# Kernel tuning notes

Measured on AMD Instinct MI355X. Metric: run time of the kernel, lower is better.

The kernel has to match this reference:

```python
import jax, jax.numpy as jnp
import numpy as np

BETA = 0.1
NUM_LAYERS = 2  # GT layers inside each FastGTN


def densify(edge_index, edge_weight, num_nodes):
    # edge_index: [T, 2, E] int, edge_weight: [T, E] -> dense [T, N, N]
    T, _, E = edge_index.shape
    t_ids = jnp.broadcast_to(jnp.arange(T)[:, None], (T, E))
    dense = jnp.zeros((T, num_nodes, num_nodes), dtype=edge_weight.dtype)
    return dense.at[t_ids, edge_index[:, 0, :], edge_index[:, 1, :]].add(edge_weight)


def fast_gtn(dense_A, X, Ws, conv_w, lin_w, lin_b, num_nodes):
    # Ws: [C, w_in, w_out]; conv_w: [L, C, T]; lin_w: [C*w_out, w_out]
    H = jnp.einsum('nk,ckh->cnh', X, Ws)              # [C, N, w_out]
    X_ = jax.lax.stop_gradient(H)                      # clone().detach()
    for l in range(NUM_LAYERS):
        filt = jax.nn.softmax(conv_w[l], axis=1)       # [C, T]
        adj = jnp.einsum('ct,tij->cij', filt, dense_A) # [C, N, N]
        H = jnp.einsum('cij,cjh->cih', adj, H)         # graph conv per channel
    H_ = jax.nn.relu(BETA * X_ + (1.0 - BETA) * H)     # [C, N, w_out]
    H_ = jnp.transpose(H_, (1, 0, 2)).reshape(num_nodes, -1)  # [N, C*w_out]
    return jax.nn.relu(H_ @ lin_w + lin_b)             # [N, w_out]


def setup_inputs() -> dict:
    key = jax.random.key(0)
    ks = jax.random.split(key, 12)
    T, E, N = 4, 131072, 4096
    C, F_IN, H_OUT = 2, 128, 64
    edge_index = jax.random.randint(ks[0], (T, 2, E), 0, N, dtype=jnp.int64)
    edge_weight = jax.random.uniform(ks[1], (T, E), dtype=jnp.float32)
    X = jax.random.normal(ks[2], (N, F_IN), dtype=jnp.float32)
    def glorot(k, shape):
        fan_in, fan_out = shape[-2], shape[-1]
        s = jnp.sqrt(6.0 / (fan_in + fan_out))
        return jax.random.uniform(k, shape, jnp.float32, -s, s)
    # FastGTN #1 (w_in=F_IN)
    Ws1 = glorot(ks[3], (C, F_IN, H_OUT))
    conv_w1 = 0.1 * jax.random.normal(ks[4], (NUM_LAYERS, C, T), dtype=jnp.float32)
    lin_w1 = glorot(ks[5], (C * H_OUT, H_OUT))
    lin_b1 = jnp.zeros((H_OUT,), jnp.float32)
    # FastGTN #2 (w_in=H_OUT)
    Ws2 = glorot(ks[6], (C, H_OUT, H_OUT))
    conv_w2 = 0.1 * jax.random.normal(ks[7], (NUM_LAYERS, C, T), dtype=jnp.float32)
    lin_w2 = glorot(ks[8], (C * H_OUT, H_OUT))
    lin_b2 = jnp.zeros((H_OUT,), jnp.float32)
    return {"edge_index": edge_index, "edge_weight": edge_weight, "X": X,
            "Ws1": Ws1, "conv_w1": conv_w1, "lin_w1": lin_w1, "lin_b1": lin_b1,
            "Ws2": Ws2, "conv_w2": conv_w2, "lin_w2": lin_w2, "lin_b2": lin_b2}


def reference(edge_index, edge_weight, X, Ws1, conv_w1, lin_w1, lin_b1,
              Ws2, conv_w2, lin_w2, lin_b2):
    N = X.shape[0]
    dense_A = densify(edge_index, edge_weight, N)      # [T, N, N]
    H = fast_gtn(dense_A, X, Ws1, conv_w1, lin_w1, lin_b1, N)
    H = fast_gtn(dense_A, H, Ws2, conv_w2, lin_w2, lin_b2, N)
    return H
```

## Files before the change

### kernel.cpp

```cpp
#include <hip/hip_runtime.h>

#define E_EDGES 131072
#define N_NODES 4096
#define HOUT    64
#define NE_TOT  (4 * E_EDGES)
#define CAP     256
#define CSTRIDE 16
#define SC_NBLK 64
#define SC_NTHR 1024
#define SC_EPB  (NE_TOT / SC_NBLK)
#define SC_EPT  (SC_EPB / SC_NTHR)

__device__ __forceinline__ unsigned short f2bf(float x) {
    unsigned u = __float_as_uint(x);
    return (unsigned short)((u + 0x7FFFu + ((u >> 16) & 1u)) >> 16);
}
__device__ __forceinline__ float bf2f(unsigned b) {
    return __uint_as_float(b << 16);
}

__device__ __forceinline__ void softmax4(const float* __restrict__ cw,
                                         int layer, int c, float f[4]) {
#pragma unroll
    for (int t = 0; t < 4; ++t) f[t] = cw[(layer * 2 + c) * 4 + t];
    float m = fmaxf(fmaxf(f[0], f[1]), fmaxf(f[2], f[3]));
    float s = 0.f;
#pragma unroll
    for (int t = 0; t < 4; ++t) { f[t] = expf(f[t] - m); s += f[t]; }
    float inv = 1.0f / s;
#pragma unroll
    for (int t = 0; t < 4; ++t) f[t] *= inv;
}

__device__ __forceinline__ float selw(const float f[4], int t) {
    float a = (t & 1) ? f[1] : f[0];
    float b = (t & 1) ? f[3] : f[2];
    return (t & 2) ? b : a;
}

__device__ __forceinline__ void fma8(float acc[8], float w, uint4 v) {
    acc[0] += w * bf2f(v.x & 0xFFFFu); acc[1] += w * bf2f(v.x >> 16);
    acc[2] += w * bf2f(v.y & 0xFFFFu); acc[3] += w * bf2f(v.y >> 16);
    acc[4] += w * bf2f(v.z & 0xFFFFu); acc[5] += w * bf2f(v.z >> 16);
    acc[6] += w * bf2f(v.w & 0xFFFFu); acc[7] += w * bf2f(v.w >> 16);
}

__device__ __forceinline__ uint4 pack8(const float acc[8]) {
    uint4 r;
    r.x = (unsigned)f2bf(acc[0]) | ((unsigned)f2bf(acc[1]) << 16);
    r.y = (unsigned)f2bf(acc[2]) | ((unsigned)f2bf(acc[3]) << 16);
    r.z = (unsigned)f2bf(acc[4]) | ((unsigned)f2bf(acc[5]) << 16);
    r.w = (unsigned)f2bf(acc[6]) | ((unsigned)f2bf(acc[7]) << 16);
    return r;
}

__device__ __forceinline__ void spmm_row2c(const unsigned* __restrict__ rowe, int len,
                                           const unsigned* __restrict__ H16,
                                           const float f0[4], const float f1[4],
                                           int lane, float a0[8], float a1[8]) {
    int g  = lane >> 3;
    int hq = lane & 7;
#pragma unroll
    for (int j = 0; j < 8; ++j) { a0[j] = 0.f; a1[j] = 0.f; }
    int e = 0;
    for (; e + 32 <= len; e += 32) {
        unsigned r0 = rowe[e + g];
        unsigned r1 = rowe[e + 8 + g];
        unsigned r2 = rowe[e + 16 + g];
        unsigned r3 = rowe[e + 24 + g];
        int   d0 = r0 & 0xFFF, t0 = (r0 >> 12) & 3;
        int   d1 = r1 & 0xFFF, t1 = (r1 >> 12) & 3;
        int   d2 = r2 & 0xFFF, t2 = (r2 >> 12) & 3;
        int   d3 = r3 & 0xFFF, t3 = (r3 >> 12) & 3;
        float w0 = bf2f(r0 >> 16), w1 = bf2f(r1 >> 16);
        float w2 = bf2f(r2 >> 16), w3 = bf2f(r3 >> 16);
        uint4 v00 = ((const uint4*)(H16 + (d0 * 2 + 0) * 32))[hq];
        uint4 v01 = ((const uint4*)(H16 + (d0 * 2 + 1) * 32))[hq];
        uint4 v10 = ((const uint4*)(H16 + (d1 * 2 + 0) * 32))[hq];
        uint4 v11 = ((const uint4*)(H16 + (d1 * 2 + 1) * 32))[hq];
        uint4 v20 = ((const uint4*)(H16 + (d2 * 2 + 0) * 32))[hq];
        uint4 v21 = ((const uint4*)(H16 + (d2 * 2 + 1) * 32))[hq];
        uint4 v30 = ((const uint4*)(H16 + (d3 * 2 + 0) * 32))[hq];
        uint4 v31 = ((const uint4*)(H16 + (d3 * 2 + 1) * 32))[hq];
        fma8(a0, w0 * selw(f0, t0), v00);
        fma8(a1, w0 * selw(f1, t0), v01);
        fma8(a0, w1 * selw(f0, t1), v10);
        fma8(a1, w1 * selw(f1, t1), v11);
        fma8(a0, w2 * selw(f0, t2), v20);
        fma8(a1, w2 * selw(f1, t2), v21);
        fma8(a0, w3 * selw(f0, t3), v30);
        fma8(a1, w3 * selw(f1, t3), v31);
    }
    for (; e + 8 <= len; e += 8) {
        unsigned r0 = rowe[e + g];
        int   d0 = r0 & 0xFFF, t0 = (r0 >> 12) & 3;
        float w0 = bf2f(r0 >> 16);
        uint4 v00 = ((const uint4*)(H16 + (d0 * 2 + 0) * 32))[hq];
        uint4 v01 = ((const uint4*)(H16 + (d0 * 2 + 1) * 32))[hq];
        fma8(a0, w0 * selw(f0, t0), v00);
        fma8(a1, w0 * selw(f1, t0), v01);
    }
    if (g < len - e) {
        unsigned r0 = rowe[e + g];
        int   d0 = r0 & 0xFFF, t0 = (r0 >> 12) & 3;
        float w0 = bf2f(r0 >> 16);
        uint4 v00 = ((const uint4*)(H16 + (d0 * 2 + 0) * 32))[hq];
        uint4 v01 = ((const uint4*)(H16 + (d0 * 2 + 1) * 32))[hq];
        fma8(a0, w0 * selw(f0, t0), v00);
        fma8(a1, w0 * selw(f1, t0), v01);
    }
#pragma unroll
    for (int j = 0; j < 8; ++j) {
        a0[j] += __shfl_xor(a0[j], 8);
        a0[j] += __shfl_xor(a0[j], 16);
        a0[j] += __shfl_xor(a0[j], 32);
        a1[j] += __shfl_xor(a1[j], 8);
        a1[j] += __shfl_xor(a1[j], 16);
        a1[j] += __shfl_xor(a1[j], 32);
    }
}

__global__ void __launch_bounds__(256)
zinit_kernel(const float* __restrict__ X, const float* __restrict__ Ws,
             float* __restrict__ H0, unsigned* __restrict__ H016,
             int* __restrict__ cursor) {
    int idx = blockIdx.x * 256 + threadIdx.x;
    if (idx < N_NODES * CSTRIDE) cursor[idx] = 0;
    int h = idx & 63;
    int n = (idx >> 6) & (N_NODES - 1);
    int c = idx >> 18;
    const float4* xv = (const float4*)(X + n * 128);
    const float*  w  = Ws + c * 128 * HOUT + h;
    float acc = 0.f;
#pragma unroll 8
    for (int k4 = 0; k4 < 32; ++k4) {
        float4 xx = xv[k4];
        acc += xx.x * w[(k4 * 4 + 0) * HOUT];
        acc += xx.y * w[(k4 * 4 + 1) * HOUT];
        acc += xx.z * w[(k4 * 4 + 2) * HOUT];
        acc += xx.w * w[(k4 * 4 + 3) * HOUT];
    }
    H0[idx] = acc;
    ((unsigned short*)H016)[(n * 2 + c) * HOUT + h] = f2bf(acc);
}

__global__ void __launch_bounds__(SC_NTHR)
scatter_kernel(const int* __restrict__ ei, const float* __restrict__ ew,
               int* __restrict__ gcursor, unsigned* __restrict__ edges) {
    __shared__ int shist[N_NODES];
    __shared__ int sbase[N_NODES];
    int tid = threadIdx.x;
    int t   = blockIdx.x >> 4;
    int e0  = (blockIdx.x & 15) * SC_EPB + tid * SC_EPT;
    const int*   ps = ei + (t * 2 + 0) * E_EDGES + e0;
    const int*   pd = ei + (t * 2 + 1) * E_EDGES + e0;
    const float* pw = ew + t * E_EDGES + e0;
#pragma unroll
    for (int j = 0; j < 4; ++j) shist[tid * 4 + j] = 0;
    __syncthreads();

    int4   s0 = ((const int4*)ps)[0],  s1 = ((const int4*)ps)[1];
    int4   d0 = ((const int4*)pd)[0],  d1 = ((const int4*)pd)[1];
    float4 w0 = ((const float4*)pw)[0], w1 = ((const float4*)pw)[1];
    int   srcs[8] = {s0.x, s0.y, s0.z, s0.w, s1.x, s1.y, s1.z, s1.w};
    int   dsts[8] = {d0.x, d0.y, d0.z, d0.w, d1.x, d1.y, d1.z, d1.w};
    float wts[8]  = {w0.x, w0.y, w0.z, w0.w, w1.x, w1.y, w1.z, w1.w};
    int lpos[8];
#pragma unroll
    for (int j = 0; j < 8; ++j) lpos[j] = atomicAdd(&shist[srcs[j]], 1);
    __syncthreads();

#pragma unroll
    for (int j = 0; j < 4; ++j) {
        int b = tid * 4 + j;
        int cntb = shist[b];
        if (cntb) sbase[b] = atomicAdd(&gcursor[b * CSTRIDE], cntb);
    }
    __syncthreads();

    unsigned tb = (unsigned)t << 12;
#pragma unroll
    for (int j = 0; j < 8; ++j) {
        unsigned p = (unsigned)(sbase[srcs[j]] + lpos[j]);
        unsigned rec = ((unsigned)f2bf(wts[j]) << 16) | tb | (unsigned)dsts[j];
        if (p < CAP) edges[srcs[j] * CAP + p] = rec;
    }
}

__global__ void __launch_bounds__(256)
spmm_kernel(const int* __restrict__ cnt, const unsigned* __restrict__ edges,
            const unsigned* __restrict__ Hin16, unsigned* __restrict__ Hout16,
            const float* __restrict__ cw) {
    int row  = (blockIdx.x * 256 + threadIdx.x) >> 6;
    int lane = threadIdx.x & 63;
    float f0[4], f1[4];
    softmax4(cw, 0, 0, f0);
    softmax4(cw, 0, 1, f1);
    int len = min(cnt[row * CSTRIDE], CAP);
    float a0[8], a1[8];
    spmm_row2c(edges + row * CAP, len, Hin16, f0, f1, lane, a0, a1);
    if ((lane >> 3) == 0) {
        int hq = lane & 7;
        ((uint4*)(Hout16 + (row * 2 + 0) * 32))[hq] = pack8(a0);
        ((uint4*)(Hout16 + (row * 2 + 1) * 32))[hq] = pack8(a1);
    }
}

template <bool FINAL>
__global__ void __launch_bounds__(256)
tail_kernel(const int* __restrict__ cnt, const unsigned* __restrict__ edges,
            const unsigned* __restrict__ Hin16,
            const float* __restrict__ H0,
            const float* __restrict__ cw,
            const float* __restrict__ lw, const float* __restrict__ lb,
            const float* __restrict__ Wsn,
            float* __restrict__ outp, unsigned* __restrict__ out16) {
    __shared__ float hcomb[4][2 * HOUT];
    __shared__ float mids[4][HOUT];
    int tid  = threadIdx.x;
    int r    = tid >> 6;
    int lane = tid & 63;
    int row  = blockIdx.x * 4 + r;

    float f0[4], f1[4];
    softmax4(cw, 1, 0, f0);
    softmax4(cw, 1, 1, f1);
    int len = min(cnt[row * CSTRIDE], CAP);
    float a0[8], a1[8];
    spmm_row2c(edges + row * CAP, len, Hin16, f0, f1, lane, a0, a1);

    if ((lane >> 3) == 0) {
        int hq = lane & 7;
#pragma unroll
        for (int j = 0; j < 8; ++j) {
            int h = hq * 8 + j;
            float h00 = H0[row * HOUT + h];
            float h01 = H0[(N_NODES + row) * HOUT + h];
            hcomb[r][h]        = fmaxf(0.1f * h00 + 0.9f * a0[j], 0.f);
            hcomb[r][HOUT + h] = fmaxf(0.1f * h01 + 0.9f * a1[j], 0.f);
        }
    }
    __syncthreads();

    float a = lb[lane];
#pragma unroll 8
    for (int j = 0; j < 2 * HOUT; ++j) a += hcomb[r][j] * lw[j * HOUT + lane];

    if (FINAL) {
        outp[row * HOUT + lane] = fmaxf(a, 0.f);
    } else {
        mids[r][lane] = fmaxf(a, 0.f);
        __syncthreads();
#pragma unroll
        for (int c = 0; c < 2; ++c) {
            float acc = 0.f;
            const float* w = Wsn + c * HOUT * HOUT + lane;
#pragma unroll 8
            for (int k = 0; k < HOUT; ++k) acc += mids[r][k] * w[k * HOUT];
            outp[(c * N_NODES + row) * HOUT + lane] = acc;
            ((unsigned short*)out16)[(row * 2 + c) * HOUT + lane] = f2bf(acc);
        }
    }
}

extern "C" void kernel_launch(void* const* d_in, const int* in_sizes, int n_in,
                              void* d_out, int out_size, void* d_ws, size_t ws_size,
                              hipStream_t stream) {
    const int*   ei  = (const int*)d_in[0];
    const float* ew  = (const float*)d_in[1];
    const float* X   = (const float*)d_in[2];
    const float* Ws1 = (const float*)d_in[3];
    const float* cw1 = (const float*)d_in[4];
    const float* lw1 = (const float*)d_in[5];
    const float* lb1 = (const float*)d_in[6];
    const float* Ws2 = (const float*)d_in[7];
    const float* cw2 = (const float*)d_in[8];
    const float* lw2 = (const float*)d_in[9];
    const float* lb2 = (const float*)d_in[10];
    float* outp = (float*)d_out;

    char* ws = (char*)d_ws;
    size_t off = 0;
    auto alloc = [&](size_t bytes) -> void* {
        void* p = ws + off;
        off += (bytes + 255) & ~size_t(255);
        return p;
    };
    int*      cursor = (int*)alloc((size_t)N_NODES * CSTRIDE * 4);
    unsigned* edges  = (unsigned*)alloc((size_t)N_NODES * CAP * 4);
    float*    H0a    = (float*)alloc((size_t)2 * N_NODES * HOUT * 4);
    unsigned* H0a16  = (unsigned*)alloc((size_t)2 * N_NODES * HOUT * 2);
    unsigned* Ha16   = (unsigned*)alloc((size_t)2 * N_NODES * HOUT * 2);
    float*    H0b    = (float*)alloc((size_t)2 * N_NODES * HOUT * 4);
    unsigned* H0b16  = (unsigned*)alloc((size_t)2 * N_NODES * HOUT * 2);

    zinit_kernel  <<<2048, 256, 0, stream>>>(X, Ws1, H0a, H0a16, cursor);
    scatter_kernel<<<SC_NBLK, SC_NTHR, 0, stream>>>(ei, ew, cursor, edges);

    spmm_kernel<<<1024, 256, 0, stream>>>(cursor, edges, H0a16, Ha16, cw1);
    tail_kernel<false><<<1024, 256, 0, stream>>>(
        cursor, edges, Ha16, H0a, cw1, lw1, lb1, Ws2, H0b, H0b16);

    spmm_kernel<<<1024, 256, 0, stream>>>(cursor, edges, H0b16, Ha16, cw2);
    tail_kernel<true><<<1024, 256, 0, stream>>>(
        cursor, edges, Ha16, H0b, cw2, lw2, lb2, nullptr, outp, nullptr);
}
```

Measured before the change: 102.1 us.

## Tile zinit projection through LDS and use nontemporal loads for SpMM gathers

```diff
diff --git a/kernel.cpp b/kernel.cpp
--- a/kernel.cpp
+++ b/kernel.cpp
@@ -11,6 +11,8 @@
 #define SC_EPB  (NE_TOT / SC_NBLK)
 #define SC_EPT  (SC_EPB / SC_NTHR)
 
+typedef unsigned uintv4 __attribute__((ext_vector_type(4)));
+
 __device__ __forceinline__ unsigned short f2bf(float x) {
     unsigned u = __float_as_uint(x);
     return (unsigned short)((u + 0x7FFFu + ((u >> 16) & 1u)) >> 16);
@@ -38,7 +40,7 @@
     return (t & 2) ? b : a;
 }
 
-__device__ __forceinline__ void fma8(float acc[8], float w, uint4 v) {
+__device__ __forceinline__ void fma8(float acc[8], float w, uintv4 v) {
     acc[0] += w * bf2f(v.x & 0xFFFFu); acc[1] += w * bf2f(v.x >> 16);
     acc[2] += w * bf2f(v.y & 0xFFFFu); acc[3] += w * bf2f(v.y >> 16);
     acc[4] += w * bf2f(v.z & 0xFFFFu); acc[5] += w * bf2f(v.z >> 16);
@@ -52,6 +54,10 @@
     r.z = (unsigned)f2bf(acc[4]) | ((unsigned)f2bf(acc[5]) << 16);
     r.w = (unsigned)f2bf(acc[6]) | ((unsigned)f2bf(acc[7]) << 16);
     return r;
+}
+
+__device__ __forceinline__ uintv4 ldnt4(const unsigned* p) {
+    return __builtin_nontemporal_load((const uintv4*)p);
 }
 
 __device__ __forceinline__ void spmm_row2c(const unsigned* __restrict__ rowe, int len,
@@ -74,14 +80,14 @@
         int   d3 = r3 & 0xFFF, t3 = (r3 >> 12) & 3;
         float w0 = bf2f(r0 >> 16), w1 = bf2f(r1 >> 16);
         float w2 = bf2f(r2 >> 16), w3 = bf2f(r3 >> 16);
-        uint4 v00 = ((const uint4*)(H16 + (d0 * 2 + 0) * 32))[hq];
-        uint4 v01 = ((const uint4*)(H16 + (d0 * 2 + 1) * 32))[hq];
-        uint4 v10 = ((const uint4*)(H16 + (d1 * 2 + 0) * 32))[hq];
-        uint4 v11 = ((const uint4*)(H16 + (d1 * 2 + 1) * 32))[hq];
-        uint4 v20 = ((const uint4*)(H16 + (d2 * 2 + 0) * 32))[hq];
-        uint4 v21 = ((const uint4*)(H16 + (d2 * 2 + 1) * 32))[hq];
-        uint4 v30 = ((const uint4*)(H16 + (d3 * 2 + 0) * 32))[hq];
-        uint4 v31 = ((const uint4*)(H16 + (d3 * 2 + 1) * 32))[hq];
+        uintv4 v00 = ldnt4(H16 + (d0 * 2 + 0) * 32 + hq * 4);
+        uintv4 v01 = ldnt4(H16 + (d0 * 2 + 1) * 32 + hq * 4);
+        uintv4 v10 = ldnt4(H16 + (d1 * 2 + 0) * 32 + hq * 4);
+        uintv4 v11 = ldnt4(H16 + (d1 * 2 + 1) * 32 + hq * 4);
+        uintv4 v20 = ldnt4(H16 + (d2 * 2 + 0) * 32 + hq * 4);
+        uintv4 v21 = ldnt4(H16 + (d2 * 2 + 1) * 32 + hq * 4);
+        uintv4 v30 = ldnt4(H16 + (d3 * 2 + 0) * 32 + hq * 4);
+        uintv4 v31 = ldnt4(H16 + (d3 * 2 + 1) * 32 + hq * 4);
         fma8(a0, w0 * selw(f0, t0), v00);
         fma8(a1, w0 * selw(f1, t0), v01);
         fma8(a0, w1 * selw(f0, t1), v10);
@@ -95,8 +101,8 @@
         unsigned r0 = rowe[e + g];
         int   d0 = r0 & 0xFFF, t0 = (r0 >> 12) & 3;
         float w0 = bf2f(r0 >> 16);
-        uint4 v00 = ((const uint4*)(H16 + (d0 * 2 + 0) * 32))[hq];
-        uint4 v01 = ((const uint4*)(H16 + (d0 * 2 + 1) * 32))[hq];
+        uintv4 v00 = ldnt4(H16 + (d0 * 2 + 0) * 32 + hq * 4);
+        uintv4 v01 = ldnt4(H16 + (d0 * 2 + 1) * 32 + hq * 4);
         fma8(a0, w0 * selw(f0, t0), v00);
         fma8(a1, w0 * selw(f1, t0), v01);
     }
@@ -104,8 +110,8 @@
         unsigned r0 = rowe[e + g];
         int   d0 = r0 & 0xFFF, t0 = (r0 >> 12) & 3;
         float w0 = bf2f(r0 >> 16);
-        uint4 v00 = ((const uint4*)(H16 + (d0 * 2 + 0) * 32))[hq];
-        uint4 v01 = ((const uint4*)(H16 + (d0 * 2 + 1) * 32))[hq];
+        uintv4 v00 = ldnt4(H16 + (d0 * 2 + 0) * 32 + hq * 4);
+        uintv4 v01 = ldnt4(H16 + (d0 * 2 + 1) * 32 + hq * 4);
         fma8(a0, w0 * selw(f0, t0), v00);
         fma8(a1, w0 * selw(f1, t0), v01);
     }
@@ -124,24 +130,49 @@
 zinit_kernel(const float* __restrict__ X, const float* __restrict__ Ws,
              float* __restrict__ H0, unsigned* __restrict__ H016,
              int* __restrict__ cursor) {
-    int idx = blockIdx.x * 256 + threadIdx.x;
-    if (idx < N_NODES * CSTRIDE) cursor[idx] = 0;
-    int h = idx & 63;
-    int n = (idx >> 6) & (N_NODES - 1);
-    int c = idx >> 18;
-    const float4* xv = (const float4*)(X + n * 128);
-    const float*  w  = Ws + c * 128 * HOUT + h;
-    float acc = 0.f;
-#pragma unroll 8
-    for (int k4 = 0; k4 < 32; ++k4) {
-        float4 xx = xv[k4];
-        acc += xx.x * w[(k4 * 4 + 0) * HOUT];
-        acc += xx.y * w[(k4 * 4 + 1) * HOUT];
-        acc += xx.z * w[(k4 * 4 + 2) * HOUT];
-        acc += xx.w * w[(k4 * 4 + 3) * HOUT];
-    }
-    H0[idx] = acc;
-    ((unsigned short*)H016)[(n * 2 + c) * HOUT + h] = f2bf(acc);
+    __shared__ float wsl[2][128][65];
+    __shared__ float xs[16][128];
+    int tid = threadIdx.x;
+    int n0  = blockIdx.x * 16;
+    cursor[blockIdx.x * 256 + tid] = 0;
+
+    for (int i = tid; i < 2 * 128 * 64; i += 256) {
+        int c = i >> 13, rem = i & 8191, k = rem >> 6, h = rem & 63;
+        wsl[c][k][h] = Ws[i];
+    }
+    for (int i4 = tid; i4 < 512; i4 += 256) {
+        int n = i4 >> 5, kq = i4 & 31;
+        ((float4*)xs[n])[kq] = ((const float4*)(X + (n0 + n) * 128))[kq];
+    }
+    __syncthreads();
+
+    int ch   = tid & 127;
+    int c    = ch >> 6, h = ch & 63;
+    int ngrp = tid >> 7;
+    float acc[8];
+#pragma unroll
+    for (int j = 0; j < 8; ++j) acc[j] = 0.f;
+#pragma unroll 4
+    for (int kq = 0; kq < 32; ++kq) {
+        float w0 = wsl[c][kq * 4 + 0][h];
+        float w1 = wsl[c][kq * 4 + 1][h];
+        float w2 = wsl[c][kq * 4 + 2][h];
+        float w3 = wsl[c][kq * 4 + 3][h];
+#pragma unroll
+        for (int j = 0; j < 8; ++j) {
+            float4 x = ((const float4*)xs[ngrp * 8 + j])[kq];
+            acc[j] += x.x * w0;
+            acc[j] += x.y * w1;
+            acc[j] += x.z * w2;
+            acc[j] += x.w * w3;
+        }
+    }
+#pragma unroll
+    for (int j = 0; j < 8; ++j) {
+        int n = n0 + ngrp * 8 + j;
+        H0[c * (N_NODES * HOUT) + n * HOUT + h] = acc[j];
+        ((unsigned short*)H016)[(n * 2 + c) * HOUT + h] = f2bf(acc[j]);
+    }
 }
 
 __global__ void __launch_bounds__(SC_NTHR)
@@ -294,7 +325,7 @@
     float*    H0b    = (float*)alloc((size_t)2 * N_NODES * HOUT * 4);
     unsigned* H0b16  = (unsigned*)alloc((size_t)2 * N_NODES * HOUT * 2);
 
-    zinit_kernel  <<<2048, 256, 0, stream>>>(X, Ws1, H0a, H0a16, cursor);
+    zinit_kernel  <<<256, 256, 0, stream>>>(X, Ws1, H0a, H0a16, cursor);
     scatter_kernel<<<SC_NBLK, SC_NTHR, 0, stream>>>(ei, ew, cursor, edges);
 
     spmm_kernel<<<1024, 256, 0, stream>>>(cursor, edges, H0a16, Ha16, cw1);
```

New measurement: 106.8 us. 1.05x slower.
